# Performance work log

Hardware: AMD Instinct MI355X
Metric: run time of the kernel (lower is better)

The kernel has to match this reference:

```python
import jax, jax.numpy as jnp
import numpy as np

NUM_COEFF = 32   # num_coeff_per_dim
NUM_POINTS = 64  # Chebyshev collocation points
MAX_ITERS = 10
TOL = 0.01
BATCH, DIM, HID, T_EVAL_N = 512, 256, 512, 16


def T_grid(t, n):
    # Chebyshev T_k(t), k=0..n-1 -> [n, len(t)]
    rows = [jnp.ones_like(t), t]
    for _ in range(2, n):
        rows.append(2.0 * t * rows[-1] - rows[-2])
    return jnp.stack(rows[:n])


def U_grid(t, n):
    rows = [jnp.ones_like(t), 2.0 * t]
    for _ in range(2, n):
        rows.append(2.0 * t * rows[-1] - rows[-2])
    return jnp.stack(rows[:n])


def DT_grid(t, n):
    # d/dt T_k = k * U_{k-1}
    return jnp.vstack([jnp.zeros((1, t.shape[0]), t.dtype),
                       U_grid(t, n - 1) * jnp.arange(1, n, dtype=t.dtype)[:, None]])


def vf_point(t, y, W1, b1, W2, b2):
    # f(t, y) for y [B, D], scalar t
    h = jnp.tanh(y @ W1 + b1 + t)
    return h @ W2 + b2


def vf_grid(t, y, W1, b1, W2, b2):
    # vectorized over Chebyshev points: y [B, D, P], t [P]
    h = jnp.tanh(jnp.einsum('bdp,dh->bhp', y, W1) + b1[None, :, None] + t[None, None, :])
    return jnp.einsum('bhp,hd->bdp', h, W2) + b2[None, :, None]


def setup_inputs() -> dict:
    key = jax.random.key(0)
    ks = jax.random.split(key, 7)
    s1 = 1.0 / np.sqrt(DIM)
    s2 = 1.0 / np.sqrt(HID)
    return {
        'y_init': jax.random.normal(ks[0], (BATCH, DIM), jnp.float32),
        't_eval': jnp.linspace(0.0, 1.0, T_EVAL_N, dtype=jnp.float32),
        'B_init': jax.random.uniform(ks[1], (BATCH, DIM, NUM_COEFF - 2), jnp.float32),
        'W1': jax.random.normal(ks[2], (DIM, HID), jnp.float32) * s1,
        'b1': jax.random.normal(ks[3], (HID,), jnp.float32) * 0.1,
        'W2': jax.random.normal(ks[4], (HID, DIM), jnp.float32) * s2,
        'b2': jax.random.normal(ks[5], (DIM,), jnp.float32) * 0.1,
    }


def _pan_solve(y_init, t_eval, B_init, W1, b1, W2, b2):
    t0, t1 = t_eval[0], t_eval[-1]
    dt = t_eval.dtype
    # time-independent spectral operators
    t_cheb = -jnp.sign(t1 - t0) * jnp.cos(jnp.pi * jnp.arange(NUM_POINTS, dtype=dt) / NUM_POINTS)
    Dt = jnp.diff(jnp.concatenate([t_cheb, jnp.ones((1,), dt)]))
    Phi = T_grid(t_cheb, NUM_COEFF)                        # [N, P]
    DPhi = (2.0 / (t1 - t0)) * DT_grid(t_cheb, NUM_COEFF)  # [N, P]
    inv0 = jnp.linalg.inv(jnp.stack([Phi[0:2, 0], DPhi[0:2, 0]]).T)  # [2,2]
    PD2 = jnp.stack([Phi[2:, 0], DPhi[2:, 0]], axis=-1)    # [N-2, 2]
    D01 = jnp.stack([DPhi[0, :], DPhi[1, :]], axis=0)      # [2, P]
    Phi_b = DPhi[2:, :] - PD2 @ inv0 @ D01                 # [N-2, P]
    Q = jnp.linalg.inv(Phi_b @ (Dt[:, None] * Phi_b.T))    # [N-2, N-2]
    PhibTQ = (Dt[:, None] * Phi_b.T) @ Q                   # [P, N-2]
    M2 = inv0 @ D01 @ PhibTQ                               # [2, N-2]

    f_init = vf_point(t0, y_init, W1, b1, W2, b2)
    yf2 = jnp.stack([y_init, f_init], axis=-1)             # [B, D, 2]

    def head(B_tail):
        return (yf2 - B_tail @ PD2) @ inv0                 # [B, D, 2]

    B = B_init
    done = jnp.array(False)
    delta = jnp.array(jnp.inf, dt)
    iters = jnp.array(0, jnp.int32)
    for _ in range(MAX_ITERS):  # Picard fixed-point iteration (masked early stop)
        B_prev = B
        B_full = jnp.concatenate([head(B_prev), B_prev], axis=-1)  # [B, D, N]
        y_grid = jnp.einsum('bdn,np->bdp', B_full, Phi)            # [B, D, P]
        fapprox = vf_grid(t_cheb, y_grid, W1, b1, W2, b2)          # [B, D, P]
        B_new = jnp.einsum('bdp,pn->bdn', fapprox, PhibTQ) - yf2 @ M2
        d = jnp.linalg.norm(B_new - B_prev)
        B = jnp.where(done, B_prev, B_new)
        delta = jnp.where(done, delta, d)
        iters = jnp.where(done, iters, iters + 1)
        done = done | (d < TOL)

    B_full = jnp.concatenate([head(B), B], axis=-1)
    t_out = -1.0 + 2.0 * (t_eval - t0) / (t1 - t0)
    Phi_out = T_grid(t_out, NUM_COEFF)                     # [N, T]
    traj = jnp.einsum('bdn,nt->tbd', B_full, Phi_out)      # [T, B, D]
    return traj, B, delta, iters


def reference(y_init, t_eval, B_init, W1, b1, W2, b2):
    traj, B, delta, iters = _pan_solve(y_init, t_eval, B_init, W1, b1, W2, b2)
    return (t_eval, traj, delta, B)
```

## Files before the change

kernel.cpp:

```cpp
#include <hip/hip_runtime.h>
#include <math.h>

#define NBATCH 512
#define NDIM 256
#define NHID 512
#define NC 32
#define NTAIL 30
#define NP 64
#define TEV 16
#define MAXIT 10
#define TOLF 0.01f
#define PI_F 3.14159265358979323846f

typedef __bf16 bf16_t;
typedef __bf16 bf16x8 __attribute__((ext_vector_type(8)));
typedef float f32x4 __attribute__((ext_vector_type(4)));
typedef unsigned short ushort_t;

constexpr size_t OFF_TCHEB = 0;
constexpr size_t OFF_PHIT  = 64;
constexpr size_t OFF_PD2I  = 2112;
constexpr size_t OFF_M2    = 2176;
constexpr size_t OFF_INV0  = 2240;
constexpr size_t OFF_PHIOUT= 2256;
constexpr size_t OFF_PQ    = 2768;
constexpr size_t OFF_PQBH  = 4816;
constexpr size_t OFF_PQBL  = 5840;
constexpr size_t OFF_PHIH  = 6864;
constexpr size_t OFF_PHIL  = 7888;
constexpr size_t OFF_SCAL  = 8912;
constexpr size_t OFF_H1F   = 8928;
constexpr size_t OFF_YF2I  = OFF_H1F + 262144;
constexpr size_t OFF_YM2   = OFF_YF2I + 262144;
constexpr size_t OFF_BT    = OFF_YM2 + 3932160;
constexpr size_t OFF_W1T   = OFF_BT + 3932160;
constexpr size_t OFF_W2T   = OFF_W1T + 65536;
constexpr size_t WS_FLOATS = OFF_W2T + 65536;

constexpr size_t OUT_TEVAL = 0;
constexpr size_t OUT_TRAJ  = 16;
constexpr size_t OUT_DELTA = 16 + (size_t)TEV*NBATCH*NDIM;
constexpr size_t OUT_B     = OUT_DELTA + 1;

__device__ __forceinline__ ushort_t bf16bits(float v) {
    bf16_t h = (bf16_t)v; ushort_t u; __builtin_memcpy(&u, &h, 2); return u;
}
__device__ __forceinline__ float bf16val(ushort_t u) {
    bf16_t h; __builtin_memcpy(&h, &u, 2); return (float)h;
}

__global__ void setup_kernel(const float* __restrict__ t_eval, float* __restrict__ ws,
                             float* __restrict__ out)
{
    __shared__ float Phi[32][64];
    __shared__ float DPhi[32][64];
    __shared__ float Phib[30][64];
    __shared__ float tcs[64];
    __shared__ float DtS[64];
    __shared__ float inv0s[4];
    __shared__ float pd2s[30][2];
    __shared__ double Gaug[30][61];
    __shared__ double rowk[60];
    __shared__ double colk[30];

    const int tid = threadIdx.x;
    const float t0 = t_eval[0], t1 = t_eval[TEV-1];
    const float sgn = (t1 > t0) ? 1.f : -1.f;

    if (tid < 64) {
        const float t = -sgn * cosf(PI_F * (float)tid / 64.f);
        tcs[tid] = t;
        float p0 = 1.f, p1 = t;
        Phi[0][tid] = p0; Phi[1][tid] = p1;
        for (int k = 2; k < 32; ++k) { float pk = 2.f*t*p1 - p0; Phi[k][tid] = pk; p0 = p1; p1 = pk; }
        const float sc = 2.f / (t1 - t0);
        float u0 = 1.f, u1 = 2.f*t;
        DPhi[0][tid] = 0.f;
        DPhi[1][tid] = sc * 1.f * u0;
        DPhi[2][tid] = sc * 2.f * u1;
        for (int k = 3; k < 32; ++k) { float uk = 2.f*t*u1 - u0; DPhi[k][tid] = sc * (float)k * uk; u0 = u1; u1 = uk; }
    }
    __syncthreads();
    if (tid < 64) DtS[tid] = ((tid < 63) ? tcs[tid+1] : 1.0f) - tcs[tid];
    if (tid == 0) {
        double a = Phi[0][0], b = DPhi[0][0], c = Phi[1][0], d = DPhi[1][0];
        double det = a*d - b*c;
        inv0s[0] = (float)( d/det); inv0s[1] = (float)(-b/det);
        inv0s[2] = (float)(-c/det); inv0s[3] = (float)( a/det);
    }
    __syncthreads();
    if (tid == 0) { ws[OFF_INV0+0]=inv0s[0]; ws[OFF_INV0+1]=inv0s[1]; ws[OFF_INV0+2]=inv0s[2]; ws[OFF_INV0+3]=inv0s[3]; }
    if (tid < 30) {
        float P = Phi[2+tid][0], D = DPhi[2+tid][0];
        float a0 = P*inv0s[0] + D*inv0s[2];
        float a1 = P*inv0s[1] + D*inv0s[3];
        pd2s[tid][0] = a0; pd2s[tid][1] = a1;
        ws[OFF_PD2I + tid*2+0] = a0;
        ws[OFF_PD2I + tid*2+1] = a1;
    }
    __syncthreads();
    if (tid < 64)
        for (int m = 0; m < 30; ++m)
            Phib[m][tid] = DPhi[2+m][tid] - (pd2s[m][0]*DPhi[0][tid] + pd2s[m][1]*DPhi[1][tid]);
    __syncthreads();

    for (int e = tid; e < 900; e += 256) {
        int i = e / 30, j = e % 30;
        double s = 0.0;
        for (int p = 0; p < 64; ++p) s += (double)Phib[i][p] * (double)DtS[p] * (double)Phib[j][p];
        Gaug[i][j] = s;
        Gaug[i][30+j] = (i == j) ? 1.0 : 0.0;
    }
    __syncthreads();

    for (int k = 0; k < 30; ++k) {
        double invpv = 1.0 / Gaug[k][k];
        if (tid < 60) rowk[tid] = Gaug[k][tid] * invpv;
        if (tid >= 64 && tid < 94) colk[tid-64] = Gaug[tid-64][k];
        __syncthreads();
        for (int e = tid; e < 1800; e += 256) {
            int i = e / 60, j = e - i*60;
            if (i == k) Gaug[i][j] = rowk[j];
            else        Gaug[i][j] -= colk[i] * rowk[j];
        }
        __syncthreads();
    }

    if (tid < 64) {
        ushort_t* pqh = (ushort_t*)(ws + OFF_PQBH);
        ushort_t* pql = (ushort_t*)(ws + OFF_PQBL);
        float pqrow[32];
        for (int n = 0; n < 30; ++n) {
            double s = 0.0;
            for (int m = 0; m < 30; ++m) s += (double)Phib[m][tid] * Gaug[m][30+n];
            pqrow[n] = (float)((double)DtS[tid] * s);
        }
        pqrow[30] = 0.f; pqrow[31] = 0.f;
        for (int n = 0; n < 32; ++n) {
            ws[OFF_PQ + (size_t)tid*32 + n] = pqrow[n];
            bf16_t h = (bf16_t)pqrow[n];
            float hf = (float)h;
            pqh[n*64 + tid] = bf16bits(pqrow[n]);
            pql[n*64 + tid] = bf16bits(pqrow[n] - hf);
        }
    }
    __syncthreads();

    if (tid < 30) {
        double a20 = 0.0, a21 = 0.0;
        for (int p = 0; p < 64; ++p) {
            double pq = (double)ws[OFF_PQ + (size_t)p*32 + tid];
            a20 += (double)DPhi[0][p] * pq;
            a21 += (double)DPhi[1][p] * pq;
        }
        ws[OFF_M2 + 0*32 + tid] = (float)((double)inv0s[0]*a20 + (double)inv0s[1]*a21);
        ws[OFF_M2 + 1*32 + tid] = (float)((double)inv0s[2]*a20 + (double)inv0s[3]*a21);
    }

    if (tid < 64) {
        ushort_t* phh = (ushort_t*)(ws + OFF_PHIH);
        ushort_t* phl = (ushort_t*)(ws + OFF_PHIL);
        for (int n = 0; n < 32; ++n) {
            float f = Phi[n][tid];
            ws[OFF_PHIT + (size_t)tid*32 + n] = f;
            ushort_t hb = bf16bits(f);
            phh[tid*32 + n] = hb;
            phl[tid*32 + n] = bf16bits(f - bf16val(hb));
        }
        ws[OFF_TCHEB + tid] = tcs[tid];
    }

    if (tid < TEV) {
        float te = t_eval[tid];
        out[OUT_TEVAL + tid] = te;
        float tt = -1.f + 2.f*(te - t0)/(t1 - t0);
        float q0 = 1.f, q1 = tt;
        ws[OFF_PHIOUT + (size_t)tid*32 + 0] = q0;
        ws[OFF_PHIOUT + (size_t)tid*32 + 1] = q1;
        for (int k = 2; k < 32; ++k) { float qk = 2.f*tt*q1 - q0; ws[OFF_PHIOUT + (size_t)tid*32 + k] = qk; q0 = q1; q1 = qk; }
    }

    if (tid == 0) {
        double* acc = (double*)(ws + OFF_SCAL);
        acc[0] = 0.0;
        int* ip = (int*)(ws + OFF_SCAL + 2);
        ip[0] = 0;
        ip[1] = 0;
    }
}

__global__ __launch_bounds__(256) void transB_kernel(const float* __restrict__ Bin, float* __restrict__ Bt)
{
    const int t = threadIdx.x, b = blockIdx.x;
    const float* src = Bin + ((size_t)(b*NDIM + t)) * NTAIL;
    #pragma unroll
    for (int n = 0; n < NTAIL; ++n)
        Bt[((size_t)b*NTAIL + n)*NDIM + t] = src[n];
}

__global__ __launch_bounds__(256) void transW_kernel(const float* __restrict__ W, bf16_t* __restrict__ Wt,
                                                     int R, int C)
{
    __shared__ float Ls[64][65];
    const int r0 = blockIdx.x*64, c0 = blockIdx.y*64;
    const int lr = threadIdx.x >> 6, lc = threadIdx.x & 63;
    #pragma unroll
    for (int i = 0; i < 16; ++i) {
        int rr = i*4 + lr;
        Ls[rr][lc] = W[(size_t)(r0+rr)*C + c0+lc];
    }
    __syncthreads();
    #pragma unroll
    for (int i = 0; i < 16; ++i) {
        int cc = i*4 + lr;
        Wt[(size_t)(c0+cc)*R + r0 + lc] = (bf16_t)Ls[lc][cc];
    }
}

__global__ __launch_bounds__(512) void finit_h_kernel(const float* __restrict__ y, const float* __restrict__ W1,
                                                      const float* __restrict__ b1, const float* __restrict__ t_eval,
                                                      float* __restrict__ h1)
{
    __shared__ float ys[NDIM];
    const int t = threadIdx.x, b = blockIdx.x;
    if (t < NDIM) ys[t] = y[(size_t)b*NDIM + t];
    __syncthreads();
    float acc = b1[t] + t_eval[0];
    for (int d = 0; d < NDIM; ++d) acc += ys[d] * W1[(size_t)d*NHID + t];
    h1[(size_t)b*NHID + t] = tanhf(acc);
}

__global__ __launch_bounds__(256) void finit_rest_kernel(const float* __restrict__ y, const float* __restrict__ W2,
                                                         const float* __restrict__ b2, const float* __restrict__ h1,
                                                         const float* __restrict__ inv0, const float* __restrict__ M2,
                                                         float* __restrict__ yf2i, float* __restrict__ yM2)
{
    __shared__ float hs[NHID];
    const int t = threadIdx.x, b = blockIdx.x;
    hs[t] = h1[(size_t)b*NHID + t];
    hs[t+256] = h1[(size_t)b*NHID + 256 + t];
    __syncthreads();
    float f = b2[t];
    for (int h = 0; h < NHID; ++h) f += hs[h] * W2[(size_t)h*NDIM + t];
    const float yv = y[(size_t)b*NDIM + t];
    yf2i[((size_t)b*2 + 0)*NDIM + t] = yv*inv0[0] + f*inv0[2];
    yf2i[((size_t)b*2 + 1)*NDIM + t] = yv*inv0[1] + f*inv0[3];
    #pragma unroll
    for (int n = 0; n < NTAIL; ++n)
        yM2[((size_t)b*NTAIL + n)*NDIM + t] = yv*M2[n] + f*M2[32 + n];
}

__global__ __launch_bounds__(512, 4) void iter_kernel(
    const float* __restrict__ pd2i, const float* __restrict__ yf2i, const float* __restrict__ tch,
    const bf16_t* __restrict__ W1t, const bf16_t* __restrict__ W2t,
    const float* __restrict__ b1f, const float* __restrict__ b2f,
    const ushort_t* __restrict__ PQhi, const ushort_t* __restrict__ PQlo,
    const ushort_t* __restrict__ phiH, const ushort_t* __restrict__ phiL,
    const float* __restrict__ yM2, float* __restrict__ Bt,
    double* __restrict__ accum, int* __restrict__ counter,
    int* __restrict__ done, float* __restrict__ outDelta)
{
    if (*done) return;
    __shared__ float pd2s[32][2];
    __shared__ float tchS[64];
    __shared__ double redd[8];
    __shared__ __align__(16) char smemA[33792];
    __shared__ __align__(16) char smemB[17408];
    __shared__ __align__(16) ushort_t PQHs[32*72];
    __shared__ __align__(16) ushort_t PQLs[32*72];

    const int t = threadIdx.x;
    const int b = blockIdx.x;
    const int lane = t & 63, w = t >> 6;
    const int fr = lane & 15, quad = lane >> 4;

    if (t < 60) ((float*)pd2s)[t] = pd2i[t];
    if (t >= 64 && t < 128) tchS[t-64] = tch[t-64];
    if (t >= 256) {
        int e = (t - 256) * 8;
        int r = e >> 6, c = e & 63;
        uint4 vh = *(const uint4*)(PQhi + e);
        uint4 vl = *(const uint4*)(PQlo + e);
        *(uint4*)(PQHs + r*72 + c) = vh;
        *(uint4*)(PQLs + r*72 + c) = vl;
    }
    __syncthreads();

    if (t < 256) {
        float cf[32];
        #pragma unroll
        for (int n = 0; n < NTAIL; ++n) cf[2+n] = Bt[((size_t)b*NTAIL + n)*NDIM + t];
        float c0 = yf2i[((size_t)b*2 + 0)*NDIM + t];
        float c1 = yf2i[((size_t)b*2 + 1)*NDIM + t];
        #pragma unroll
        for (int n = 0; n < NTAIL; ++n) { c0 -= cf[2+n]*pd2s[n][0]; c1 -= cf[2+n]*pd2s[n][1]; }
        cf[0] = c0; cf[1] = c1;
        unsigned* BH32 = (unsigned*)smemA;
        unsigned* BL32 = (unsigned*)(smemA + 16384);
        #pragma unroll
        for (int n2 = 0; n2 < 16; ++n2) {
            float f0 = cf[2*n2], f1 = cf[2*n2+1];
            ushort_t h0 = bf16bits(f0), h1 = bf16bits(f1);
            ushort_t l0 = bf16bits(f0 - bf16val(h0)), l1 = bf16bits(f1 - bf16val(h1));
            int idx = t*16 + ((n2 >> 2) ^ (t & 3))*4 + (n2 & 3);
            BH32[idx] = (unsigned)h0 | ((unsigned)h1 << 16);
            BL32[idx] = (unsigned)l0 | ((unsigned)l1 << 16);
        }
    }
    __syncthreads();

    ushort_t* Ay = (ushort_t*)smemA;
    {
        bf16x8 bH[2], bL[2];
        const ushort_t* BHu = (const ushort_t*)smemA;
        const ushort_t* BLu = (const ushort_t*)(smemA + 16384);
        #pragma unroll
        for (int j = 0; j < 2; ++j) {
            const int d = w*32 + j*16 + fr;
            const int off = d*32 + (quad ^ (d & 3))*8;
            bH[j] = *(const bf16x8*)(BHu + off);
            bL[j] = *(const bf16x8*)(BLu + off);
        }
        bf16x8 aH[4], aL[4];
        #pragma unroll
        for (int i = 0; i < 4; ++i) {
            aH[i] = *(const bf16x8*)(phiH + (i*16 + fr)*32 + quad*8);
            aL[i] = *(const bf16x8*)(phiL + (i*16 + fr)*32 + quad*8);
        }
        __syncthreads();
        f32x4 accY[4][2];
        #pragma unroll
        for (int i = 0; i < 4; ++i)
            #pragma unroll
            for (int j = 0; j < 2; ++j) {
                f32x4 a = (f32x4){0.f,0.f,0.f,0.f};
                a = __builtin_amdgcn_mfma_f32_16x16x32_bf16(aH[i], bH[j], a, 0, 0, 0);
                a = __builtin_amdgcn_mfma_f32_16x16x32_bf16(aH[i], bL[j], a, 0, 0, 0);
                a = __builtin_amdgcn_mfma_f32_16x16x32_bf16(aL[i], bH[j], a, 0, 0, 0);
                accY[i][j] = a;
            }
        #pragma unroll
        for (int i = 0; i < 4; ++i)
            #pragma unroll
            for (int j = 0; j < 2; ++j)
                #pragma unroll
                for (int r = 0; r < 4; ++r) {
                    const int p = i*16 + quad*4 + r;
                    const int d = w*32 + j*16 + fr;
                    Ay[p*264 + d] = bf16bits(accY[i][j][r]);
                }
    }
    __syncthreads();

    ushort_t* Hc = (ushort_t*)smemB;
    f32x4 accF[4][2];
    #pragma unroll
    for (int i = 0; i < 4; ++i)
        #pragma unroll
        for (int j = 0; j < 2; ++j) accF[i][j] = (f32x4){0.f,0.f,0.f,0.f};

    #pragma unroll
    for (int pass = 0; pass < 4; ++pass) {
        bf16x8 w2f[4][2];
        #pragma unroll
        for (int kt4 = 0; kt4 < 4; ++kt4)
            #pragma unroll
            for (int j = 0; j < 2; ++j) {
                const int d = w*32 + j*16 + fr;
                w2f[kt4][j] = *(const bf16x8*)(W2t + (size_t)d*NHID + pass*128 + kt4*32 + quad*8);
            }
        f32x4 acc1[4];
        #pragma unroll
        for (int i = 0; i < 4; ++i) acc1[i] = (f32x4){0.f,0.f,0.f,0.f};
        #pragma unroll
        for (int kt = 0; kt < NDIM; kt += 32) {
            bf16x8 af[4], bfv;
            #pragma unroll
            for (int i = 0; i < 4; ++i)
                af[i] = *(const bf16x8*)(Ay + (i*16 + fr)*264 + kt + quad*8);
            {
                const int ncol = pass*128 + w*16 + fr;
                bfv = *(const bf16x8*)(W1t + (size_t)ncol*NDIM + kt + quad*8);
            }
            #pragma unroll
            for (int i = 0; i < 4; ++i)
                acc1[i] = __builtin_amdgcn_mfma_f32_16x16x32_bf16(af[i], bfv, acc1[i], 0, 0, 0);
        }
        __syncthreads();
        {
            const int col = w*16 + fr;
            const float bv = b1f[pass*128 + col];
            #pragma unroll
            for (int i = 0; i < 4; ++i)
                #pragma unroll
                for (int r = 0; r < 4; ++r) {
                    const int row = i*16 + quad*4 + r;
                    float v = acc1[i][r] + bv + tchS[row];
                    v = fminf(fmaxf(v, -15.f), 15.f);
                    float e = __expf(2.f*v);
                    Hc[row*136 + col] = bf16bits((e - 1.f)/(e + 1.f));
                }
        }
        __syncthreads();
        #pragma unroll
        for (int kt4 = 0; kt4 < 4; ++kt4) {
            bf16x8 af[4];
            #pragma unroll
            for (int i = 0; i < 4; ++i)
                af[i] = *(const bf16x8*)(Hc + (i*16 + fr)*136 + kt4*32 + quad*8);
            #pragma unroll
            for (int i = 0; i < 4; ++i)
                #pragma unroll
                for (int j = 0; j < 2; ++j)
                    accF[i][j] = __builtin_amdgcn_mfma_f32_16x16x32_bf16(af[i], w2f[kt4][j], accF[i][j], 0, 0, 0);
        }
    }
    __syncthreads();

    {
        unsigned* FsT32 = (unsigned*)smemA;
        #pragma unroll
        for (int i = 0; i < 4; ++i)
            #pragma unroll
            for (int j = 0; j < 2; ++j) {
                const int d = w*32 + j*16 + fr;
                const float bv = b2f[d];
                #pragma unroll
                for (int rp = 0; rp < 2; ++rp) {
                    unsigned u0 = bf16bits(accF[i][j][rp*2]   + bv);
                    unsigned u1 = bf16bits(accF[i][j][rp*2+1] + bv);
                    FsT32[d*33 + i*8 + quad*2 + rp] = u0 | (u1 << 16);
                }
            }
    }
    __syncthreads();

    double ss = 0.0;
    {
        const ushort_t* FsTu = (const ushort_t*)smemA;
        f32x4 acc2[2][2];
        #pragma unroll
        for (int m2 = 0; m2 < 2; ++m2)
            #pragma unroll
            for (int j2 = 0; j2 < 2; ++j2) acc2[m2][j2] = (f32x4){0.f,0.f,0.f,0.f};
        #pragma unroll
        for (int kk = 0; kk < 2; ++kk) {
            bf16x8 ah[2], al[2];
            #pragma unroll
            for (int m2 = 0; m2 < 2; ++m2) {
                const int off = (m2*16 + fr)*72 + kk*32 + quad*8;
                ah[m2] = *(const bf16x8*)(PQHs + off);
                al[m2] = *(const bf16x8*)(PQLs + off);
            }
            #pragma unroll
            for (int j2 = 0; j2 < 2; ++j2) {
                const int d2 = w*32 + j2*16 + fr;
                bf16x8 bfv = *(const bf16x8*)(FsTu + d2*66 + kk*32 + quad*8);
                #pragma unroll
                for (int m2 = 0; m2 < 2; ++m2) {
                    acc2[m2][j2] = __builtin_amdgcn_mfma_f32_16x16x32_bf16(ah[m2], bfv, acc2[m2][j2], 0, 0, 0);
                    acc2[m2][j2] = __builtin_amdgcn_mfma_f32_16x16x32_bf16(al[m2], bfv, acc2[m2][j2], 0, 0, 0);
                }
            }
        }
        #pragma unroll
        for (int m2 = 0; m2 < 2; ++m2)
            #pragma unroll
            for (int j2 = 0; j2 < 2; ++j2)
                #pragma unroll
                for (int rr = 0; rr < 4; ++rr) {
                    const int n = m2*16 + quad*4 + rr;
                    if (n < NTAIL) {
                        const int d = w*32 + j2*16 + fr;
                        const size_t idx = ((size_t)b*NTAIL + n)*NDIM + d;
                        float val = acc2[m2][j2][rr] - yM2[idx];
                        float old = Bt[idx];
                        float diff = val - old;
                        Bt[idx] = val;
                        ss += (double)diff*(double)diff;
                    }
                }
    }

    #pragma unroll
    for (int off = 32; off > 0; off >>= 1) ss += __shfl_down(ss, off, 64);
    if (lane == 0) redd[w] = ss;
    __syncthreads();
    if (t == 0) {
        double tot = redd[0] + redd[1] + redd[2] + redd[3]
                   + redd[4] + redd[5] + redd[6] + redd[7];
        atomicAdd(accum, tot);
        __threadfence();
        int old = atomicAdd(counter, 1);
        if (old == 511) {
            unsigned long long raw = atomicExch((unsigned long long*)accum, 0ull);
            double total; __builtin_memcpy(&total, &raw, 8);
            float dl = (float)sqrt(total);
            *outDelta = dl;
            *counter = 0;
            if (dl < TOLF) *done = 1;
        }
    }
}

__global__ __launch_bounds__(256) void kernelEpi(const float* __restrict__ PhiOut, const float* __restrict__ pd2i,
                                                 const float* __restrict__ yf2i, const float* __restrict__ Bt,
                                                 float* __restrict__ outTraj, float* __restrict__ outB)
{
    __shared__ float Po[16][32];
    const int t = threadIdx.x, b = blockIdx.x;
    for (int i = t; i < 512; i += 256) ((float*)Po)[i] = PhiOut[i];
    __syncthreads();
    float cf[32];
    #pragma unroll
    for (int n = 0; n < NTAIL; ++n) cf[2+n] = Bt[((size_t)b*NTAIL + n)*NDIM + t];
    float c0 = yf2i[((size_t)b*2 + 0)*NDIM + t];
    float c1 = yf2i[((size_t)b*2 + 1)*NDIM + t];
    #pragma unroll
    for (int n = 0; n < NTAIL; ++n) { c0 -= cf[2+n]*pd2i[n*2]; c1 -= cf[2+n]*pd2i[n*2+1]; }
    cf[0] = c0; cf[1] = c1;
    for (int tt = 0; tt < TEV; ++tt) {
        float s = 0.f;
        #pragma unroll
        for (int k = 0; k < 32; ++k) s += cf[k]*Po[tt][k];
        outTraj[((size_t)tt*NBATCH + b)*NDIM + t] = s;
    }
    float* ob = outB + ((size_t)(b*NDIM + t))*NTAIL;
    #pragma unroll
    for (int n = 0; n < NTAIL; ++n) ob[n] = cf[2+n];
}

extern "C" void kernel_launch(void* const* d_in, const int* in_sizes, int n_in,
                              void* d_out, int out_size, void* d_ws, size_t ws_size,
                              hipStream_t stream)
{
    const float* y_init = (const float*)d_in[0];
    const float* t_eval = (const float*)d_in[1];
    const float* B_init = (const float*)d_in[2];
    const float* W1     = (const float*)d_in[3];
    const float* b1     = (const float*)d_in[4];
    const float* W2     = (const float*)d_in[5];
    const float* b2     = (const float*)d_in[6];
    float* out = (float*)d_out;
    float* ws  = (float*)d_ws;
    if (ws_size < WS_FLOATS * sizeof(float)) return;

    float* tcheb = ws + OFF_TCHEB;
    float* pd2i  = ws + OFF_PD2I;
    float* M2    = ws + OFF_M2;
    float* inv0  = ws + OFF_INV0;
    float* PhiOut= ws + OFF_PHIOUT;
    double* accum = (double*)(ws + OFF_SCAL);
    int* done    = (int*)(ws + OFF_SCAL + 2);
    int* counter = (int*)(ws + OFF_SCAL + 3);
    float* h1   = ws + OFF_H1F;
    float* yf2i = ws + OFF_YF2I;
    float* yM2  = ws + OFF_YM2;
    float* Bt   = ws + OFF_BT;
    bf16_t* W1t = (bf16_t*)(ws + OFF_W1T);
    bf16_t* W2t = (bf16_t*)(ws + OFF_W2T);
    ushort_t* pqh = (ushort_t*)(ws + OFF_PQBH);
    ushort_t* pql = (ushort_t*)(ws + OFF_PQBL);
    ushort_t* phh = (ushort_t*)(ws + OFF_PHIH);
    ushort_t* phl = (ushort_t*)(ws + OFF_PHIL);

    setup_kernel<<<1, 256, 0, stream>>>(t_eval, ws, out);
    transB_kernel<<<NBATCH, 256, 0, stream>>>(B_init, Bt);
    transW_kernel<<<dim3(NDIM/64, NHID/64), 256, 0, stream>>>(W1, W1t, NDIM, NHID);
    transW_kernel<<<dim3(NHID/64, NDIM/64), 256, 0, stream>>>(W2, W2t, NHID, NDIM);
    finit_h_kernel<<<NBATCH, 512, 0, stream>>>(y_init, W1, b1, t_eval, h1);
    finit_rest_kernel<<<NBATCH, 256, 0, stream>>>(y_init, W2, b2, h1, inv0, M2, yf2i, yM2);

    for (int it = 0; it < MAXIT; ++it) {
        iter_kernel<<<NBATCH, 512, 0, stream>>>(pd2i, yf2i, tcheb, W1t, W2t, b1, b2,
                                                pqh, pql, phh, phl, yM2, Bt,
                                                accum, counter, done, out + OUT_DELTA);
    }
    kernelEpi<<<NBATCH, 256, 0, stream>>>(PhiOut, pd2i, yf2i, Bt, out + OUT_TRAJ, out + OUT_B);
}
```

Baseline: 736.1 us.

## Double-buffer tanh hidden tile and overlap second GEMM with next pass

```diff
diff --git a/kernel.cpp b/kernel.cpp
--- a/kernel.cpp
+++ b/kernel.cpp
@@ -265,9 +265,7 @@
     __shared__ float tchS[64];
     __shared__ double redd[8];
     __shared__ __align__(16) char smemA[33792];
-    __shared__ __align__(16) char smemB[17408];
-    __shared__ __align__(16) ushort_t PQHs[32*72];
-    __shared__ __align__(16) ushort_t PQLs[32*72];
+    __shared__ __align__(16) char smemB[2][17408];
 
     const int t = threadIdx.x;
     const int b = blockIdx.x;
@@ -276,14 +274,6 @@
 
     if (t < 60) ((float*)pd2s)[t] = pd2i[t];
     if (t >= 64 && t < 128) tchS[t-64] = tch[t-64];
-    if (t >= 256) {
-        int e = (t - 256) * 8;
-        int r = e >> 6, c = e & 63;
-        uint4 vh = *(const uint4*)(PQhi + e);
-        uint4 vl = *(const uint4*)(PQlo + e);
-        *(uint4*)(PQHs + r*72 + c) = vh;
-        *(uint4*)(PQLs + r*72 + c) = vl;
-    }
     __syncthreads();
 
     if (t < 256) {
@@ -352,7 +342,6 @@
     }
     __syncthreads();
 
-    ushort_t* Hc = (ushort_t*)smemB;
     f32x4 accF[4][2];
     #pragma unroll
     for (int i = 0; i < 4; ++i)
@@ -361,14 +350,26 @@
 
     #pragma unroll
     for (int pass = 0; pass < 4; ++pass) {
-        bf16x8 w2f[4][2];
-        #pragma unroll
-        for (int kt4 = 0; kt4 < 4; ++kt4)
-            #pragma unroll
-            for (int j = 0; j < 2; ++j) {
-                const int d = w*32 + j*16 + fr;
-                w2f[kt4][j] = *(const bf16x8*)(W2t + (size_t)d*NHID + pass*128 + kt4*32 + quad*8);
-            }
+        if (pass > 0) {
+            const ushort_t* HcR = (const ushort_t*)smemB[(pass-1) & 1];
+            #pragma unroll
+            for (int kt4 = 0; kt4 < 4; ++kt4) {
+                bf16x8 afh[4], w2f[2];
+                #pragma unroll
+                for (int i = 0; i < 4; ++i)
+                    afh[i] = *(const bf16x8*)(HcR + (i*16 + fr)*136 + kt4*32 + quad*8);
+                #pragma unroll
+                for (int j = 0; j < 2; ++j) {
+                    const int d = w*32 + j*16 + fr;
+                    w2f[j] = *(const bf16x8*)(W2t + (size_t)d*NHID + (pass-1)*128 + kt4*32 + quad*8);
+                }
+                #pragma unroll
+                for (int i = 0; i < 4; ++i)
+                    #pragma unroll
+                    for (int j = 0; j < 2; ++j)
+                        accF[i][j] = __builtin_amdgcn_mfma_f32_16x16x32_bf16(afh[i], w2f[j], accF[i][j], 0, 0, 0);
+            }
+        }
         f32x4 acc1[4];
         #pragma unroll
         for (int i = 0; i < 4; ++i) acc1[i] = (f32x4){0.f,0.f,0.f,0.f};
@@ -386,8 +387,8 @@
             for (int i = 0; i < 4; ++i)
                 acc1[i] = __builtin_amdgcn_mfma_f32_16x16x32_bf16(af[i], bfv, acc1[i], 0, 0, 0);
         }
-        __syncthreads();
         {
+            ushort_t* HcW = (ushort_t*)smemB[pass & 1];
             const int col = w*16 + fr;
             const float bv = b1f[pass*128 + col];
             #pragma unroll
@@ -398,24 +399,31 @@
                     float v = acc1[i][r] + bv + tchS[row];
                     v = fminf(fmaxf(v, -15.f), 15.f);
                     float e = __expf(2.f*v);
-                    Hc[row*136 + col] = bf16bits((e - 1.f)/(e + 1.f));
+                    HcW[row*136 + col] = bf16bits((e - 1.f)/(e + 1.f));
                 }
         }
         __syncthreads();
+    }
+    {
+        const ushort_t* HcR = (const ushort_t*)smemB[1];
         #pragma unroll
         for (int kt4 = 0; kt4 < 4; ++kt4) {
-            bf16x8 af[4];
+            bf16x8 afh[4], w2f[2];
             #pragma unroll
             for (int i = 0; i < 4; ++i)
-                af[i] = *(const bf16x8*)(Hc + (i*16 + fr)*136 + kt4*32 + quad*8);
+                afh[i] = *(const bf16x8*)(HcR + (i*16 + fr)*136 + kt4*32 + quad*8);
+            #pragma unroll
+            for (int j = 0; j < 2; ++j) {
+                const int d = w*32 + j*16 + fr;
+                w2f[j] = *(const bf16x8*)(W2t + (size_t)d*NHID + 3*128 + kt4*32 + quad*8);
+            }
             #pragma unroll
             for (int i = 0; i < 4; ++i)
                 #pragma unroll
                 for (int j = 0; j < 2; ++j)
-                    accF[i][j] = __builtin_amdgcn_mfma_f32_16x16x32_bf16(af[i], w2f[kt4][j], accF[i][j], 0, 0, 0);
-        }
-    }
-    __syncthreads();
+                    accF[i][j] = __builtin_amdgcn_mfma_f32_16x16x32_bf16(afh[i], w2f[j], accF[i][j], 0, 0, 0);
+        }
+    }
 
     {
         unsigned* FsT32 = (unsigned*)smemA;
@@ -448,9 +456,9 @@
             bf16x8 ah[2], al[2];
             #pragma unroll
             for (int m2 = 0; m2 < 2; ++m2) {
-                const int off = (m2*16 + fr)*72 + kk*32 + quad*8;
-                ah[m2] = *(const bf16x8*)(PQHs + off);
-                al[m2] = *(const bf16x8*)(PQLs + off);
+                const int goff = (m2*16 + fr)*64 + kk*32 + quad*8;
+                ah[m2] = *(const bf16x8*)(PQhi + goff);
+                al[m2] = *(const bf16x8*)(PQlo + goff);
             }
             #pragma unroll
             for (int j2 = 0; j2 < 2; ++j2) {
```

Measured after the change: 790.1 us. 7.3% more time.

## Fuse Picard iterations and epilogue into one cooperative persistent kernel

Applied to the files above, without the earlier changes.

```diff
diff --git a/kernel.cpp b/kernel.cpp
--- a/kernel.cpp
+++ b/kernel.cpp
@@ -1,5 +1,8 @@
 #include <hip/hip_runtime.h>
+#include <hip/hip_cooperative_groups.h>
 #include <math.h>
+
+namespace cg = cooperative_groups;
 
 #define NBATCH 512
 #define NDIM 256
@@ -35,7 +38,8 @@
 constexpr size_t OFF_BT    = OFF_YM2 + 3932160;
 constexpr size_t OFF_W1T   = OFF_BT + 3932160;
 constexpr size_t OFF_W2T   = OFF_W1T + 65536;
-constexpr size_t WS_FLOATS = OFF_W2T + 65536;
+constexpr size_t OFF_ACC   = OFF_W2T + 65536;
+constexpr size_t WS_FLOATS = OFF_ACC + 32;
 
 constexpr size_t OUT_TEVAL = 0;
 constexpr size_t OUT_TRAJ  = 16;
@@ -187,6 +191,7 @@
         ip[0] = 0;
         ip[1] = 0;
     }
+    if (tid < 16) ((double*)(ws + OFF_ACC))[tid] = 0.0;
 }
 
 __global__ __launch_bounds__(256) void transB_kernel(const float* __restrict__ Bin, float* __restrict__ Bt)
@@ -248,6 +253,287 @@
     #pragma unroll
     for (int n = 0; n < NTAIL; ++n)
         yM2[((size_t)b*NTAIL + n)*NDIM + t] = yv*M2[n] + f*M2[32 + n];
+}
+
+__global__ __launch_bounds__(512, 4) void iter_persist(
+    const float* __restrict__ pd2i, const float* __restrict__ yf2i, const float* __restrict__ tch,
+    const bf16_t* __restrict__ W1t, const bf16_t* __restrict__ W2t,
+    const float* __restrict__ b1f, const float* __restrict__ b2f,
+    const ushort_t* __restrict__ PQhi, const ushort_t* __restrict__ PQlo,
+    const ushort_t* __restrict__ phiH, const ushort_t* __restrict__ phiL,
+    const float* __restrict__ yM2, float* __restrict__ Bt,
+    double* __restrict__ accArr, float* __restrict__ outDelta,
+    const float* __restrict__ PhiOut, float* __restrict__ outTraj, float* __restrict__ outB)
+{
+    cg::grid_group grid = cg::this_grid();
+
+    __shared__ float pd2s[32][2];
+    __shared__ float tchS[64];
+    __shared__ double redd[8];
+    __shared__ __align__(16) char smemA[33792];
+    __shared__ __align__(16) char smemB[17408];
+    __shared__ __align__(16) ushort_t PQHs[32*72];
+    __shared__ __align__(16) ushort_t PQLs[32*72];
+
+    const int t = threadIdx.x;
+    const int b = blockIdx.x;
+    const int lane = t & 63, w = t >> 6;
+    const int fr = lane & 15, quad = lane >> 4;
+
+    if (t < 60) ((float*)pd2s)[t] = pd2i[t];
+    if (t >= 64 && t < 128) tchS[t-64] = tch[t-64];
+    if (t >= 256) {
+        int e = (t - 256) * 8;
+        int r = e >> 6, c = e & 63;
+        uint4 vh = *(const uint4*)(PQhi + e);
+        uint4 vl = *(const uint4*)(PQlo + e);
+        *(uint4*)(PQHs + r*72 + c) = vh;
+        *(uint4*)(PQLs + r*72 + c) = vl;
+    }
+
+    float dl = 1e30f;
+    for (int it = 0; it < MAXIT; ++it) {
+        __syncthreads();
+
+        if (t < 256) {
+            float cf[32];
+            #pragma unroll
+            for (int n = 0; n < NTAIL; ++n) cf[2+n] = Bt[((size_t)b*NTAIL + n)*NDIM + t];
+            float c0 = yf2i[((size_t)b*2 + 0)*NDIM + t];
+            float c1 = yf2i[((size_t)b*2 + 1)*NDIM + t];
+            #pragma unroll
+            for (int n = 0; n < NTAIL; ++n) { c0 -= cf[2+n]*pd2s[n][0]; c1 -= cf[2+n]*pd2s[n][1]; }
+            cf[0] = c0; cf[1] = c1;
+            unsigned* BH32 = (unsigned*)smemA;
+            unsigned* BL32 = (unsigned*)(smemA + 16384);
+            #pragma unroll
+            for (int n2 = 0; n2 < 16; ++n2) {
+                float f0 = cf[2*n2], f1 = cf[2*n2+1];
+                ushort_t h0 = bf16bits(f0), h1 = bf16bits(f1);
+                ushort_t l0 = bf16bits(f0 - bf16val(h0)), l1 = bf16bits(f1 - bf16val(h1));
+                int idx = t*16 + ((n2 >> 2) ^ (t & 3))*4 + (n2 & 3);
+                BH32[idx] = (unsigned)h0 | ((unsigned)h1 << 16);
+                BL32[idx] = (unsigned)l0 | ((unsigned)l1 << 16);
+            }
+        }
+        __syncthreads();
+
+        ushort_t* Ay = (ushort_t*)smemA;
+        {
+            bf16x8 bH[2], bL[2];
+            const ushort_t* BHu = (const ushort_t*)smemA;
+            const ushort_t* BLu = (const ushort_t*)(smemA + 16384);
+            #pragma unroll
+            for (int j = 0; j < 2; ++j) {
+                const int d = w*32 + j*16 + fr;
+                const int off = d*32 + (quad ^ (d & 3))*8;
+                bH[j] = *(const bf16x8*)(BHu + off);
+                bL[j] = *(const bf16x8*)(BLu + off);
+            }
+            bf16x8 aH[4], aL[4];
+            #pragma unroll
+            for (int i = 0; i < 4; ++i) {
+                aH[i] = *(const bf16x8*)(phiH + (i*16 + fr)*32 + quad*8);
+                aL[i] = *(const bf16x8*)(phiL + (i*16 + fr)*32 + quad*8);
+            }
+            __syncthreads();
+            f32x4 accY[4][2];
+            #pragma unroll
+            for (int i = 0; i < 4; ++i)
+                #pragma unroll
+                for (int j = 0; j < 2; ++j) {
+                    f32x4 a = (f32x4){0.f,0.f,0.f,0.f};
+                    a = __builtin_amdgcn_mfma_f32_16x16x32_bf16(aH[i], bH[j], a, 0, 0, 0);
+                    a = __builtin_amdgcn_mfma_f32_16x16x32_bf16(aH[i], bL[j], a, 0, 0, 0);
+                    a = __builtin_amdgcn_mfma_f32_16x16x32_bf16(aL[i], bH[j], a, 0, 0, 0);
+                    accY[i][j] = a;
+                }
+            #pragma unroll
+            for (int i = 0; i < 4; ++i)
+                #pragma unroll
+                for (int j = 0; j < 2; ++j)
+                    #pragma unroll
+                    for (int r = 0; r < 4; ++r) {
+                        const int p = i*16 + quad*4 + r;
+                        const int d = w*32 + j*16 + fr;
+                        Ay[p*264 + d] = bf16bits(accY[i][j][r]);
+                    }
+        }
+        __syncthreads();
+
+        ushort_t* Hc = (ushort_t*)smemB;
+        f32x4 accF[4][2];
+        #pragma unroll
+        for (int i = 0; i < 4; ++i)
+            #pragma unroll
+            for (int j = 0; j < 2; ++j) accF[i][j] = (f32x4){0.f,0.f,0.f,0.f};
+
+        #pragma unroll
+        for (int pass = 0; pass < 4; ++pass) {
+            bf16x8 w2f[4][2];
+            #pragma unroll
+            for (int kt4 = 0; kt4 < 4; ++kt4)
+                #pragma unroll
+                for (int j = 0; j < 2; ++j) {
+                    const int d = w*32 + j*16 + fr;
+                    w2f[kt4][j] = *(const bf16x8*)(W2t + (size_t)d*NHID + pass*128 + kt4*32 + quad*8);
+                }
+            f32x4 acc1[4];
+            #pragma unroll
+            for (int i = 0; i < 4; ++i) acc1[i] = (f32x4){0.f,0.f,0.f,0.f};
+            #pragma unroll
+            for (int kt = 0; kt < NDIM; kt += 32) {
+                bf16x8 af[4], bfv;
+                #pragma unroll
+                for (int i = 0; i < 4; ++i)
+                    af[i] = *(const bf16x8*)(Ay + (i*16 + fr)*264 + kt + quad*8);
+                {
+                    const int ncol = pass*128 + w*16 + fr;
+                    bfv = *(const bf16x8*)(W1t + (size_t)ncol*NDIM + kt + quad*8);
+                }
+                #pragma unroll
+                for (int i = 0; i < 4; ++i)
+                    acc1[i] = __builtin_amdgcn_mfma_f32_16x16x32_bf16(af[i], bfv, acc1[i], 0, 0, 0);
+            }
+            __syncthreads();
+            {
+                const int col = w*16 + fr;
+                const float bv = b1f[pass*128 + col];
+                #pragma unroll
+                for (int i = 0; i < 4; ++i)
+                    #pragma unroll
+                    for (int r = 0; r < 4; ++r) {
+                        const int row = i*16 + quad*4 + r;
+                        float v = acc1[i][r] + bv + tchS[row];
+                        v = fminf(fmaxf(v, -15.f), 15.f);
+                        float e = __expf(2.f*v);
+                        Hc[row*136 + col] = bf16bits((e - 1.f)/(e + 1.f));
+                    }
+            }
+            __syncthreads();
+            #pragma unroll
+            for (int kt4 = 0; kt4 < 4; ++kt4) {
+                bf16x8 af[4];
+                #pragma unroll
+                for (int i = 0; i < 4; ++i)
+                    af[i] = *(const bf16x8*)(Hc + (i*16 + fr)*136 + kt4*32 + quad*8);
+                #pragma unroll
+                for (int i = 0; i < 4; ++i)
+                    #pragma unroll
+                    for (int j = 0; j < 2; ++j)
+                        accF[i][j] = __builtin_amdgcn_mfma_f32_16x16x32_bf16(af[i], w2f[kt4][j], accF[i][j], 0, 0, 0);
+            }
+        }
+        __syncthreads();
+
+        {
+            unsigned* FsT32 = (unsigned*)smemA;
+            #pragma unroll
+            for (int i = 0; i < 4; ++i)
+                #pragma unroll
+                for (int j = 0; j < 2; ++j) {
+                    const int d = w*32 + j*16 + fr;
+                    const float bv = b2f[d];
+                    #pragma unroll
+                    for (int rp = 0; rp < 2; ++rp) {
+                        unsigned u0 = bf16bits(accF[i][j][rp*2]   + bv);
+                        unsigned u1 = bf16bits(accF[i][j][rp*2+1] + bv);
+                        FsT32[d*33 + i*8 + quad*2 + rp] = u0 | (u1 << 16);
+                    }
+                }
+        }
+        __syncthreads();
+
+        double ss = 0.0;
+        {
+            const ushort_t* FsTu = (const ushort_t*)smemA;
+            f32x4 acc2[2][2];
+            #pragma unroll
+            for (int m2 = 0; m2 < 2; ++m2)
+                #pragma unroll
+                for (int j2 = 0; j2 < 2; ++j2) acc2[m2][j2] = (f32x4){0.f,0.f,0.f,0.f};
+            #pragma unroll
+            for (int kk = 0; kk < 2; ++kk) {
+                bf16x8 ah[2], al[2];
+                #pragma unroll
+                for (int m2 = 0; m2 < 2; ++m2) {
+                    const int off = (m2*16 + fr)*72 + kk*32 + quad*8;
+                    ah[m2] = *(const bf16x8*)(PQHs + off);
+                    al[m2] = *(const bf16x8*)(PQLs + off);
+                }
+                #pragma unroll
+                for (int j2 = 0; j2 < 2; ++j2) {
+                    const int d2 = w*32 + j2*16 + fr;
+                    bf16x8 bfv = *(const bf16x8*)(FsTu + d2*66 + kk*32 + quad*8);
+                    #pragma unroll
+                    for (int m2 = 0; m2 < 2; ++m2) {
+                        acc2[m2][j2] = __builtin_amdgcn_mfma_f32_16x16x32_bf16(ah[m2], bfv, acc2[m2][j2], 0, 0, 0);
+                        acc2[m2][j2] = __builtin_amdgcn_mfma_f32_16x16x32_bf16(al[m2], bfv, acc2[m2][j2], 0, 0, 0);
+                    }
+                }
+            }
+            #pragma unroll
+            for (int m2 = 0; m2 < 2; ++m2)
+                #pragma unroll
+                for (int j2 = 0; j2 < 2; ++j2)
+                    #pragma unroll
+                    for (int rr = 0; rr < 4; ++rr) {
+                        const int n = m2*16 + quad*4 + rr;
+                        if (n < NTAIL) {
+                            const int d = w*32 + j2*16 + fr;
+                            const size_t idx = ((size_t)b*NTAIL + n)*NDIM + d;
+                            float val = acc2[m2][j2][rr] - yM2[idx];
+                            float old = Bt[idx];
+                            float diff = val - old;
+                            Bt[idx] = val;
+                            ss += (double)diff*(double)diff;
+                        }
+                    }
+        }
+
+        #pragma unroll
+        for (int off = 32; off > 0; off >>= 1) ss += __shfl_down(ss, off, 64);
+        if (lane == 0) redd[w] = ss;
+        __syncthreads();
+        if (t == 0) {
+            double tot = redd[0] + redd[1] + redd[2] + redd[3]
+                       + redd[4] + redd[5] + redd[6] + redd[7];
+            atomicAdd(&accArr[it], tot);
+            __threadfence();
+        }
+        grid.sync();
+        double total = *((volatile double*)&accArr[it]);
+        dl = (float)sqrt(total);
+        if (b == 0 && t == 0) *outDelta = dl;
+        if (dl < TOLF) break;
+    }
+
+    __syncthreads();
+    {
+        float* Po = (float*)smemB;
+        if (t < 512) { if (t < 512) Po[t] = PhiOut[t]; }
+    }
+    __syncthreads();
+    if (t < 256) {
+        const float* Po = (const float*)smemB;
+        float cf[32];
+        #pragma unroll
+        for (int n = 0; n < NTAIL; ++n) cf[2+n] = Bt[((size_t)b*NTAIL + n)*NDIM + t];
+        float c0 = yf2i[((size_t)b*2 + 0)*NDIM + t];
+        float c1 = yf2i[((size_t)b*2 + 1)*NDIM + t];
+        #pragma unroll
+        for (int n = 0; n < NTAIL; ++n) { c0 -= cf[2+n]*pd2s[n][0]; c1 -= cf[2+n]*pd2s[n][1]; }
+        cf[0] = c0; cf[1] = c1;
+        for (int tt = 0; tt < TEV; ++tt) {
+            float s = 0.f;
+            #pragma unroll
+            for (int k = 0; k < 32; ++k) s += cf[k]*Po[tt*32 + k];
+            outTraj[((size_t)tt*NBATCH + b)*NDIM + t] = s;
+        }
+        float* ob = outB + ((size_t)(b*NDIM + t))*NTAIL;
+        #pragma unroll
+        for (int n = 0; n < NTAIL; ++n) ob[n] = cf[2+n];
+    }
 }
 
 __global__ __launch_bounds__(512, 4) void iter_kernel(
@@ -495,10 +781,10 @@
         if (old == 511) {
             unsigned long long raw = atomicExch((unsigned long long*)accum, 0ull);
             double total; __builtin_memcpy(&total, &raw, 8);
-            float dl = (float)sqrt(total);
-            *outDelta = dl;
+            float dlv = (float)sqrt(total);
+            *outDelta = dlv;
             *counter = 0;
-            if (dl < TOLF) *done = 1;
+            if (dlv < TOLF) *done = 1;
         }
     }
 }
@@ -553,6 +839,7 @@
     double* accum = (double*)(ws + OFF_SCAL);
     int* done    = (int*)(ws + OFF_SCAL + 2);
     int* counter = (int*)(ws + OFF_SCAL + 3);
+    double* accArr = (double*)(ws + OFF_ACC);
     float* h1   = ws + OFF_H1F;
     float* yf2i = ws + OFF_YF2I;
     float* yM2  = ws + OFF_YM2;
@@ -563,6 +850,9 @@
     ushort_t* pql = (ushort_t*)(ws + OFF_PQBL);
     ushort_t* phh = (ushort_t*)(ws + OFF_PHIH);
     ushort_t* phl = (ushort_t*)(ws + OFF_PHIL);
+    float* outDeltaP = out + OUT_DELTA;
+    float* outTrajP  = out + OUT_TRAJ;
+    float* outBP     = out + OUT_B;
 
     setup_kernel<<<1, 256, 0, stream>>>(t_eval, ws, out);
     transB_kernel<<<NBATCH, 256, 0, stream>>>(B_init, Bt);
@@ -571,10 +861,32 @@
     finit_h_kernel<<<NBATCH, 512, 0, stream>>>(y_init, W1, b1, t_eval, h1);
     finit_rest_kernel<<<NBATCH, 256, 0, stream>>>(y_init, W2, b2, h1, inv0, M2, yf2i, yM2);
 
-    for (int it = 0; it < MAXIT; ++it) {
-        iter_kernel<<<NBATCH, 512, 0, stream>>>(pd2i, yf2i, tcheb, W1t, W2t, b1, b2,
-                                                pqh, pql, phh, phl, yM2, Bt,
-                                                accum, counter, done, out + OUT_DELTA);
-    }
-    kernelEpi<<<NBATCH, 256, 0, stream>>>(PhiOut, pd2i, yf2i, Bt, out + OUT_TRAJ, out + OUT_B);
-}
+    const bf16_t* W1tc = W1t; const bf16_t* W2tc = W2t;
+    const float* pd2ic = pd2i; const float* yf2ic = yf2i; const float* tchc = tcheb;
+    const float* b1c = b1; const float* b2c = b2;
+    const ushort_t* pqhc = pqh; const ushort_t* pqlc = pql;
+    const ushort_t* phhc = phh; const ushort_t* phlc = phl;
+    const float* yM2c = yM2; const float* PhiOutc = PhiOut;
+
+    void* kargs[] = {
+        (void*)&pd2ic, (void*)&yf2ic, (void*)&tchc,
+        (void*)&W1tc, (void*)&W2tc,
+        (void*)&b1c, (void*)&b2c,
+        (void*)&pqhc, (void*)&pqlc,
+        (void*)&phhc, (void*)&phlc,
+        (void*)&yM2c, (void*)&Bt,
+        (void*)&accArr, (void*)&outDeltaP,
+        (void*)&PhiOutc, (void*)&outTrajP, (void*)&outBP
+    };
+    hipError_t cerr = hipLaunchCooperativeKernel((const void*)iter_persist,
+                                                 dim3(NBATCH), dim3(512),
+                                                 kargs, 0, stream);
+    if (cerr != hipSuccess) {
+        for (int it = 0; it < MAXIT; ++it) {
+            iter_kernel<<<NBATCH, 512, 0, stream>>>(pd2i, yf2i, tcheb, W1t, W2t, b1, b2,
+                                                    pqh, pql, phh, phl, yM2, Bt,
+                                                    accum, counter, done, outDeltaP);
+        }
+        kernelEpi<<<NBATCH, 256, 0, stream>>>(PhiOut, pd2i, yf2i, Bt, outTrajP, outBP);
+    }
+}
```

Result: slower. 2.142 ms (+191.0%).

## Double iter_kernel block to 1024 threads, one 16-column tile per wave

Applied to the files above, without the earlier changes.

```diff
diff --git a/kernel.cpp b/kernel.cpp
--- a/kernel.cpp
+++ b/kernel.cpp
@@ -250,7 +250,7 @@
         yM2[((size_t)b*NTAIL + n)*NDIM + t] = yv*M2[n] + f*M2[32 + n];
 }
 
-__global__ __launch_bounds__(512, 4) void iter_kernel(
+__global__ __launch_bounds__(1024, 8) void iter_kernel(
     const float* __restrict__ pd2i, const float* __restrict__ yf2i, const float* __restrict__ tch,
     const bf16_t* __restrict__ W1t, const bf16_t* __restrict__ W2t,
     const float* __restrict__ b1f, const float* __restrict__ b2f,
@@ -263,9 +263,9 @@
     if (*done) return;
     __shared__ float pd2s[32][2];
     __shared__ float tchS[64];
-    __shared__ double redd[8];
+    __shared__ double redd[16];
     __shared__ __align__(16) char smemA[33792];
-    __shared__ __align__(16) char smemB[17408];
+    __shared__ __align__(16) char smemB[33792];
     __shared__ __align__(16) ushort_t PQHs[32*72];
     __shared__ __align__(16) ushort_t PQLs[32*72];
 
@@ -273,10 +273,11 @@
     const int b = blockIdx.x;
     const int lane = t & 63, w = t >> 6;
     const int fr = lane & 15, quad = lane >> 4;
+    const int dcol = w*16 + fr;
 
     if (t < 60) ((float*)pd2s)[t] = pd2i[t];
     if (t >= 64 && t < 128) tchS[t-64] = tch[t-64];
-    if (t >= 256) {
+    if (t >= 256 && t < 512) {
         int e = (t - 256) * 8;
         int r = e >> 6, c = e & 63;
         uint4 vh = *(const uint4*)(PQhi + e);
@@ -311,15 +312,13 @@
 
     ushort_t* Ay = (ushort_t*)smemA;
     {
-        bf16x8 bH[2], bL[2];
+        bf16x8 bH, bL;
         const ushort_t* BHu = (const ushort_t*)smemA;
         const ushort_t* BLu = (const ushort_t*)(smemA + 16384);
-        #pragma unroll
-        for (int j = 0; j < 2; ++j) {
-            const int d = w*32 + j*16 + fr;
-            const int off = d*32 + (quad ^ (d & 3))*8;
-            bH[j] = *(const bf16x8*)(BHu + off);
-            bL[j] = *(const bf16x8*)(BLu + off);
+        {
+            const int off = dcol*32 + (quad ^ (dcol & 3))*8;
+            bH = *(const bf16x8*)(BHu + off);
+            bL = *(const bf16x8*)(BLu + off);
         }
         bf16x8 aH[4], aL[4];
         #pragma unroll
@@ -328,47 +327,36 @@
             aL[i] = *(const bf16x8*)(phiL + (i*16 + fr)*32 + quad*8);
         }
         __syncthreads();
-        f32x4 accY[4][2];
+        f32x4 accY[4];
+        #pragma unroll
+        for (int i = 0; i < 4; ++i) {
+            f32x4 a = (f32x4){0.f,0.f,0.f,0.f};
+            a = __builtin_amdgcn_mfma_f32_16x16x32_bf16(aH[i], bH, a, 0, 0, 0);
+            a = __builtin_amdgcn_mfma_f32_16x16x32_bf16(aH[i], bL, a, 0, 0, 0);
+            a = __builtin_amdgcn_mfma_f32_16x16x32_bf16(aL[i], bH, a, 0, 0, 0);
+            accY[i] = a;
+        }
         #pragma unroll
         for (int i = 0; i < 4; ++i)
             #pragma unroll
-            for (int j = 0; j < 2; ++j) {
-                f32x4 a = (f32x4){0.f,0.f,0.f,0.f};
-                a = __builtin_amdgcn_mfma_f32_16x16x32_bf16(aH[i], bH[j], a, 0, 0, 0);
-                a = __builtin_amdgcn_mfma_f32_16x16x32_bf16(aH[i], bL[j], a, 0, 0, 0);
-                a = __builtin_amdgcn_mfma_f32_16x16x32_bf16(aL[i], bH[j], a, 0, 0, 0);
-                accY[i][j] = a;
+            for (int r = 0; r < 4; ++r) {
+                const int p = i*16 + quad*4 + r;
+                Ay[p*264 + dcol] = bf16bits(accY[i][r]);
             }
-        #pragma unroll
-        for (int i = 0; i < 4; ++i)
-            #pragma unroll
-            for (int j = 0; j < 2; ++j)
-                #pragma unroll
-                for (int r = 0; r < 4; ++r) {
-                    const int p = i*16 + quad*4 + r;
-                    const int d = w*32 + j*16 + fr;
-                    Ay[p*264 + d] = bf16bits(accY[i][j][r]);
-                }
     }
     __syncthreads();
 
     ushort_t* Hc = (ushort_t*)smemB;
-    f32x4 accF[4][2];
-    #pragma unroll
-    for (int i = 0; i < 4; ++i)
-        #pragma unroll
-        for (int j = 0; j < 2; ++j) accF[i][j] = (f32x4){0.f,0.f,0.f,0.f};
-
-    #pragma unroll
-    for (int pass = 0; pass < 4; ++pass) {
-        bf16x8 w2f[4][2];
-        #pragma unroll
-        for (int kt4 = 0; kt4 < 4; ++kt4)
-            #pragma unroll
-            for (int j = 0; j < 2; ++j) {
-                const int d = w*32 + j*16 + fr;
-                w2f[kt4][j] = *(const bf16x8*)(W2t + (size_t)d*NHID + pass*128 + kt4*32 + quad*8);
-            }
+    f32x4 accF[4];
+    #pragma unroll
+    for (int i = 0; i < 4; ++i) accF[i] = (f32x4){0.f,0.f,0.f,0.f};
+
+    #pragma unroll
+    for (int pass = 0; pass < 2; ++pass) {
+        bf16x8 w2f[8];
+        #pragma unroll
+        for (int kt4 = 0; kt4 < 8; ++kt4)
+            w2f[kt4] = *(const bf16x8*)(W2t + (size_t)dcol*NHID + pass*256 + kt4*32 + quad*8);
         f32x4 acc1[4];
         #pragma unroll
         for (int i = 0; i < 4; ++i) acc1[i] = (f32x4){0.f,0.f,0.f,0.f};
@@ -379,7 +367,7 @@
             for (int i = 0; i < 4; ++i)
                 af[i] = *(const bf16x8*)(Ay + (i*16 + fr)*264 + kt + quad*8);
             {
-                const int ncol = pass*128 + w*16 + fr;
+                const int ncol = pass*256 + w*16 + fr;
                 bfv = *(const bf16x8*)(W1t + (size_t)ncol*NDIM + kt + quad*8);
             }
             #pragma unroll
@@ -389,7 +377,7 @@
         __syncthreads();
         {
             const int col = w*16 + fr;
-            const float bv = b1f[pass*128 + col];
+            const float bv = b1f[pass*256 + col];
             #pragma unroll
             for (int i = 0; i < 4; ++i)
                 #pragma unroll
@@ -398,39 +386,33 @@
                     float v = acc1[i][r] + bv + tchS[row];
                     v = fminf(fmaxf(v, -15.f), 15.f);
                     float e = __expf(2.f*v);
-                    Hc[row*136 + col] = bf16bits((e - 1.f)/(e + 1.f));
+                    Hc[row*264 + col] = bf16bits((e - 1.f)/(e + 1.f));
                 }
         }
         __syncthreads();
         #pragma unroll
-        for (int kt4 = 0; kt4 < 4; ++kt4) {
+        for (int kt4 = 0; kt4 < 8; ++kt4) {
             bf16x8 af[4];
             #pragma unroll
             for (int i = 0; i < 4; ++i)
-                af[i] = *(const bf16x8*)(Hc + (i*16 + fr)*136 + kt4*32 + quad*8);
+                af[i] = *(const bf16x8*)(Hc + (i*16 + fr)*264 + kt4*32 + quad*8);
             #pragma unroll
             for (int i = 0; i < 4; ++i)
-                #pragma unroll
-                for (int j = 0; j < 2; ++j)
-                    accF[i][j] = __builtin_amdgcn_mfma_f32_16x16x32_bf16(af[i], w2f[kt4][j], accF[i][j], 0, 0, 0);
+                accF[i] = __builtin_amdgcn_mfma_f32_16x16x32_bf16(af[i], w2f[kt4], accF[i], 0, 0, 0);
         }
     }
     __syncthreads();
 
     {
         unsigned* FsT32 = (unsigned*)smemA;
+        const float bv = b2f[dcol];
         #pragma unroll
         for (int i = 0; i < 4; ++i)
             #pragma unroll
-            for (int j = 0; j < 2; ++j) {
-                const int d = w*32 + j*16 + fr;
-                const float bv = b2f[d];
-                #pragma unroll
-                for (int rp = 0; rp < 2; ++rp) {
-                    unsigned u0 = bf16bits(accF[i][j][rp*2]   + bv);
-                    unsigned u1 = bf16bits(accF[i][j][rp*2+1] + bv);
-                    FsT32[d*33 + i*8 + quad*2 + rp] = u0 | (u1 << 16);
-                }
+            for (int rp = 0; rp < 2; ++rp) {
+                unsigned u0 = bf16bits(accF[i][rp*2]   + bv);
+                unsigned u1 = bf16bits(accF[i][rp*2+1] + bv);
+                FsT32[dcol*33 + i*8 + quad*2 + rp] = u0 | (u1 << 16);
             }
     }
     __syncthreads();
@@ -438,11 +420,9 @@
     double ss = 0.0;
     {
         const ushort_t* FsTu = (const ushort_t*)smemA;
-        f32x4 acc2[2][2];
-        #pragma unroll
-        for (int m2 = 0; m2 < 2; ++m2)
-            #pragma unroll
-            for (int j2 = 0; j2 < 2; ++j2) acc2[m2][j2] = (f32x4){0.f,0.f,0.f,0.f};
+        f32x4 acc2[2];
+        #pragma unroll
+        for (int m2 = 0; m2 < 2; ++m2) acc2[m2] = (f32x4){0.f,0.f,0.f,0.f};
         #pragma unroll
         for (int kk = 0; kk < 2; ++kk) {
             bf16x8 ah[2], al[2];
@@ -452,34 +432,27 @@
                 ah[m2] = *(const bf16x8*)(PQHs + off);
                 al[m2] = *(const bf16x8*)(PQLs + off);
             }
-            #pragma unroll
-            for (int j2 = 0; j2 < 2; ++j2) {
-                const int d2 = w*32 + j2*16 + fr;
-                bf16x8 bfv = *(const bf16x8*)(FsTu + d2*66 + kk*32 + quad*8);
-                #pragma unroll
-                for (int m2 = 0; m2 < 2; ++m2) {
-                    acc2[m2][j2] = __builtin_amdgcn_mfma_f32_16x16x32_bf16(ah[m2], bfv, acc2[m2][j2], 0, 0, 0);
-                    acc2[m2][j2] = __builtin_amdgcn_mfma_f32_16x16x32_bf16(al[m2], bfv, acc2[m2][j2], 0, 0, 0);
+            bf16x8 bfv = *(const bf16x8*)(FsTu + dcol*66 + kk*32 + quad*8);
+            #pragma unroll
+            for (int m2 = 0; m2 < 2; ++m2) {
+                acc2[m2] = __builtin_amdgcn_mfma_f32_16x16x32_bf16(ah[m2], bfv, acc2[m2], 0, 0, 0);
+                acc2[m2] = __builtin_amdgcn_mfma_f32_16x16x32_bf16(al[m2], bfv, acc2[m2], 0, 0, 0);
+            }
+        }
+        #pragma unroll
+        for (int m2 = 0; m2 < 2; ++m2)
+            #pragma unroll
+            for (int rr = 0; rr < 4; ++rr) {
+                const int n = m2*16 + quad*4 + rr;
+                if (n < NTAIL) {
+                    const size_t idx = ((size_t)b*NTAIL + n)*NDIM + dcol;
+                    float val = acc2[m2][rr] - yM2[idx];
+                    float old = Bt[idx];
+                    float diff = val - old;
+                    Bt[idx] = val;
+                    ss += (double)diff*(double)diff;
                 }
             }
-        }
-        #pragma unroll
-        for (int m2 = 0; m2 < 2; ++m2)
-            #pragma unroll
-            for (int j2 = 0; j2 < 2; ++j2)
-                #pragma unroll
-                for (int rr = 0; rr < 4; ++rr) {
-                    const int n = m2*16 + quad*4 + rr;
-                    if (n < NTAIL) {
-                        const int d = w*32 + j2*16 + fr;
-                        const size_t idx = ((size_t)b*NTAIL + n)*NDIM + d;
-                        float val = acc2[m2][j2][rr] - yM2[idx];
-                        float old = Bt[idx];
-                        float diff = val - old;
-                        Bt[idx] = val;
-                        ss += (double)diff*(double)diff;
-                    }
-                }
     }
 
     #pragma unroll
@@ -487,8 +460,9 @@
     if (lane == 0) redd[w] = ss;
     __syncthreads();
     if (t == 0) {
-        double tot = redd[0] + redd[1] + redd[2] + redd[3]
-                   + redd[4] + redd[5] + redd[6] + redd[7];
+        double tot = 0.0;
+        #pragma unroll
+        for (int i = 0; i < 16; ++i) tot += redd[i];
         atomicAdd(accum, tot);
         __threadfence();
         int old = atomicAdd(counter, 1);
@@ -572,9 +546,9 @@
     finit_rest_kernel<<<NBATCH, 256, 0, stream>>>(y_init, W2, b2, h1, inv0, M2, yf2i, yM2);
 
     for (int it = 0; it < MAXIT; ++it) {
-        iter_kernel<<<NBATCH, 512, 0, stream>>>(pd2i, yf2i, tcheb, W1t, W2t, b1, b2,
-                                                pqh, pql, phh, phl, yM2, Bt,
-                                                accum, counter, done, out + OUT_DELTA);
+        iter_kernel<<<NBATCH, 1024, 0, stream>>>(pd2i, yf2i, tcheb, W1t, W2t, b1, b2,
+                                                 pqh, pql, phh, phl, yM2, Bt,
+                                                 accum, counter, done, out + OUT_DELTA);
     }
     kernelEpi<<<NBATCH, 256, 0, stream>>>(PhiOut, pd2i, yf2i, Bt, out + OUT_TRAJ, out + OUT_B);
 }
```

Measured after the change: 1.019 ms. 1.38x slower.
